# Kernel optimization log

Measured on AMD Instinct MI355X. Metric: run time of the kernel, lower is better.

Reference implementation:

```python
import jax, jax.numpy as jnp
import numpy as np

HIDDEN = 4096
N_HEADS = 16
HEAD_DIM = HIDDEN // N_HEADS  # 256
ROTARY_DIM = 64
MAX_POS = 2048
INIT_RANGE = 0.02


def _create_sinusoidal_positions(num_pos, dim):
    inv_freq = 1.0 / 10000 ** (np.arange(0, dim, 2) / dim)
    sinusoid_inp = np.einsum('i,j->ij', np.arange(num_pos), inv_freq).astype('float32')
    sin, cos = np.sin(sinusoid_inp), np.cos(sinusoid_inp)
    sentinel = dim // 2 + dim % 2
    out = np.zeros((num_pos, dim), dtype=np.float32)
    out[:, :sentinel] = sin
    out[:, sentinel:] = cos
    return jnp.array(out)

EMBED_POSITIONS = _create_sinusoidal_positions(MAX_POS, ROTARY_DIM)  # [MAX_POS, ROTARY_DIM]


def _rotate_every_two(t):
    # t: [B,S,H,R] -> interleaved (-x1, x0, -x3, x2, ...)
    rot = jnp.stack((-t[..., 1::2], t[..., ::2]), axis=-1)
    return rot.reshape(rot.shape[:-2] + (-1,))


def _apply_rotary(t, sin, cos):
    # sin/cos: [B,S,R/2] -> element-wise repeat x2 along last axis -> [B,S,1,R]
    sin_p = jnp.repeat(sin[:, :, None, :], 2, axis=-1)
    cos_p = jnp.repeat(cos[:, :, None, :], 2, axis=-1)
    return t * cos_p + _rotate_every_two(t) * sin_p


def setup_inputs() -> dict:
    key = jax.random.key(0)
    k0, k1, k2, k3, k4 = jax.random.split(key, 5)
    B, S = 2, 2048
    hidden_states = jax.random.normal(k0, (B, S, HIDDEN), dtype=jnp.float32)
    attention_mask = jnp.ones((B, S), dtype=jnp.float32)
    position_ids = jnp.broadcast_to(jnp.arange(S, dtype=jnp.int32), (B, S))
    Wq = jax.random.normal(k1, (HIDDEN, HIDDEN), dtype=jnp.float32) * INIT_RANGE
    Wk = jax.random.normal(k2, (HIDDEN, HIDDEN), dtype=jnp.float32) * INIT_RANGE
    Wv = jax.random.normal(k3, (HIDDEN, HIDDEN), dtype=jnp.float32) * INIT_RANGE
    Wo = jax.random.normal(k4, (HIDDEN, HIDDEN), dtype=jnp.float32) * INIT_RANGE
    return {"hidden_states": hidden_states, "attention_mask": attention_mask,
            "position_ids": position_ids, "Wq": Wq, "Wk": Wk, "Wv": Wv, "Wo": Wo}


def reference(hidden_states, attention_mask, position_ids, Wq, Wk, Wv, Wo):
    B, S, _ = hidden_states.shape
    # QKV projections (no bias), split heads -> [B,S,H,D]
    q = (hidden_states @ Wq).reshape(B, S, N_HEADS, HEAD_DIM)
    k = (hidden_states @ Wk).reshape(B, S, N_HEADS, HEAD_DIM)
    v = (hidden_states @ Wv).reshape(B, S, N_HEADS, HEAD_DIM)

    sincos = jnp.take(EMBED_POSITIONS, position_ids, axis=0)  # [B,S,ROTARY_DIM]
    sin, cos = jnp.split(sincos, 2, axis=-1)

    # Interleaved RoPE on first ROTARY_DIM channels only
    q_rot = _apply_rotary(q[..., :ROTARY_DIM], sin, cos)
    k_rot = _apply_rotary(k[..., :ROTARY_DIM], sin, cos)
    q = jnp.concatenate([q_rot, q[..., ROTARY_DIM:]], axis=-1)
    k = jnp.concatenate([k_rot, k[..., ROTARY_DIM:]], axis=-1)

    # Combined causal + padding mask -> additive bias
    causal = jnp.tril(jnp.ones((S, S), dtype=bool))[None, None]          # [1,1,S,S]
    pad = (attention_mask > 0)[:, None, None, :]                          # [B,1,1,S]
    mask = causal & pad                                                    # [B,1,S,S]
    bias = jnp.where(mask, 0.0, jnp.finfo(jnp.float32).min).astype(jnp.float32)

    # Scaled dot-product attention (query pre-scaled, as in flax dpa_weights)
    q = q / jnp.sqrt(jnp.float32(HEAD_DIM))
    scores = jnp.einsum('bqhd,bkhd->bhqk', q, k) + bias
    attn = jax.nn.softmax(scores, axis=-1)
    out = jnp.einsum('bhqk,bkhd->bqhd', attn, v).reshape(B, S, HIDDEN)
    return out @ Wo
```

## Files before the change

### kernel.cpp

```cpp
#include <hip/hip_runtime.h>


typedef unsigned short u16;
typedef __attribute__((ext_vector_type(4))) float f32x4;
typedef __attribute__((ext_vector_type(8))) short s16x8;
typedef __attribute__((ext_vector_type(4))) unsigned short u16x4;

#define HID 4096
#define SEQ 2048
#define NMAT (4096ull * 4096ull)

__device__ __forceinline__ u16 f2bf(float x) {
  unsigned int u = __builtin_bit_cast(unsigned int, x);
  u += 0x7FFFu + ((u >> 16) & 1u);
  return (u16)(u >> 16);
}
__device__ __forceinline__ float bf2f(u16 x) {
  unsigned int u = ((unsigned int)x) << 16;
  return __builtin_bit_cast(float, u);
}
__device__ __forceinline__ void cp16(const void* g, void* l) {
  __builtin_amdgcn_global_load_lds((__attribute__((address_space(1))) void*)(g),
                                   (__attribute__((address_space(3))) void*)(l),
                                   16, 0, 0);
}

__global__ __launch_bounds__(256) void k_cvt(const float* __restrict__ src,
                                             u16* __restrict__ dst) {
  size_t i = ((size_t)blockIdx.x * 256 + threadIdx.x) * 8;
  f32x4 a = *(const f32x4*)(src + i);
  f32x4 b = *(const f32x4*)(src + i + 4);
  u16x4 o0, o1;
  o0[0] = f2bf(a[0]); o0[1] = f2bf(a[1]); o0[2] = f2bf(a[2]); o0[3] = f2bf(a[3]);
  o1[0] = f2bf(b[0]); o1[1] = f2bf(b[1]); o1[2] = f2bf(b[2]); o1[3] = f2bf(b[3]);
  *(u16x4*)(dst + i) = o0;
  *(u16x4*)(dst + i + 4) = o1;
}

__global__ __launch_bounds__(256) void k_wtrans(const float* __restrict__ W0,
                                                const float* __restrict__ W1,
                                                const float* __restrict__ W2,
                                                const float* __restrict__ W3,
                                                u16* __restrict__ WT) {
  int z = blockIdx.z;
  const float* W = (z == 0) ? W0 : (z == 1) ? W1 : (z == 2) ? W2 : W3;
  u16* T = WT + (size_t)z * NMAT;
  __shared__ u16 tile[64][70];
  int t = threadIdx.x, tx = t & 15, ty = t >> 4;
  int n0 = blockIdx.x * 64, k0 = blockIdx.y * 64;
  for (int i = 0; i < 4; i++) {
    int kl = ty + 16 * i;
    f32x4 v = *(const f32x4*)(W + (size_t)(k0 + kl) * HID + n0 + tx * 4);
    tile[kl][tx * 4 + 0] = f2bf(v[0]);
    tile[kl][tx * 4 + 1] = f2bf(v[1]);
    tile[kl][tx * 4 + 2] = f2bf(v[2]);
    tile[kl][tx * 4 + 3] = f2bf(v[3]);
  }
  __syncthreads();
  for (int i = 0; i < 4; i++) {
    int nl = ty + 16 * i;
    u16x4 o;
    o[0] = tile[tx * 4 + 0][nl];
    o[1] = tile[tx * 4 + 1][nl];
    o[2] = tile[tx * 4 + 2][nl];
    o[3] = tile[tx * 4 + 3][nl];
    *(u16x4*)(T + (size_t)(n0 + nl) * HID + k0 + tx * 4) = o;
  }
}

__global__ __launch_bounds__(256) void k_vtrans(const u16* __restrict__ V,
                                                u16* __restrict__ Vt) {
  int bh = blockIdx.z, b = bh >> 4, h = bh & 15;
  int tok0 = blockIdx.x * 64, d0 = blockIdx.y * 64;
  __shared__ u16 tile[64][70];
  int t = threadIdx.x, tx = t & 15, ty = t >> 4;
  for (int i = 0; i < 4; i++) {
    int tl = ty + 16 * i;
    u16x4 v = *(const u16x4*)(V + (size_t)(b * SEQ + tok0 + tl) * HID + h * 256 + d0 + tx * 4);
    tile[tl][tx * 4 + 0] = v[0];
    tile[tl][tx * 4 + 1] = v[1];
    tile[tl][tx * 4 + 2] = v[2];
    tile[tl][tx * 4 + 3] = v[3];
  }
  __syncthreads();
  for (int i = 0; i < 4; i++) {
    int dl = ty + 16 * i;
    u16x4 o;
    o[0] = tile[tx * 4 + 0][dl];
    o[1] = tile[tx * 4 + 1][dl];
    o[2] = tile[tx * 4 + 2][dl];
    o[3] = tile[tx * 4 + 3][dl];
    *(u16x4*)(Vt + ((size_t)bh * 256 + d0 + dl) * SEQ + tok0 + tx * 4) = o;
  }
}

template <bool QKV>
__global__ __launch_bounds__(256) void k_gemm(const u16* __restrict__ A,
                                              const u16* __restrict__ Bt0,
                                              u16* __restrict__ Cb0,
                                              float* __restrict__ Cf) {
  const int t = threadIdx.x, lane = t & 63, w = t >> 6;
  const int bm = blockIdx.y * 128, bn = blockIdx.x * 128;
  const u16* Bt = Bt0;
  u16* Cb = Cb0;
  float scale = 1.f;
  if (QKV) {
    int z = blockIdx.z;
    Bt += (size_t)z * NMAT;
    Cb += (size_t)z * NMAT;
    if (z == 0) scale = 0.0625f;
  }
  __shared__ u16 As[4096];
  __shared__ u16 Bs[4096];
  int r = t >> 2, cs0 = t & 3, cg = cs0 ^ ((r >> 1) & 3);
  const u16* ga = A + (size_t)(bm + r) * HID + cg * 8;
  const u16* gb = Bt + (size_t)(bn + r) * HID + cg * 8;
  u16* la = As + w * 512;
  u16* lb = Bs + w * 512;
  const int wm = (w >> 1) * 64, wn = (w & 1) * 64;
  const u16* ra[4];
  const u16* rb[4];
  for (int mi = 0; mi < 4; mi++) {
    int row = wm + mi * 16 + (lane & 15);
    int cs = (lane >> 4) ^ ((row >> 1) & 3);
    ra[mi] = As + row * 32 + cs * 8;
  }
  for (int ni = 0; ni < 4; ni++) {
    int row = wn + ni * 16 + (lane & 15);
    int cs = (lane >> 4) ^ ((row >> 1) & 3);
    rb[ni] = Bs + row * 32 + cs * 8;
  }
  f32x4 acc[4][4] = {};
  for (int k0 = 0; k0 < HID; k0 += 32) {
    __syncthreads();
    cp16(ga, la);
    cp16(ga + 64 * HID, la + 2048);
    cp16(gb, lb);
    cp16(gb + 64 * HID, lb + 2048);
    ga += 32;
    gb += 32;
    __syncthreads();
    s16x8 af[4], bf[4];
    for (int mi = 0; mi < 4; mi++) af[mi] = *(const s16x8*)ra[mi];
    for (int ni = 0; ni < 4; ni++) bf[ni] = *(const s16x8*)rb[ni];
    for (int mi = 0; mi < 4; mi++)
      for (int ni = 0; ni < 4; ni++)
        acc[mi][ni] = __builtin_amdgcn_mfma_f32_16x16x32_bf16(af[mi], bf[ni], acc[mi][ni], 0, 0, 0);
  }
  for (int mi = 0; mi < 4; mi++)
    for (int ni = 0; ni < 4; ni++) {
      int ml = bm + wm + mi * 16 + ((lane >> 4) << 2);
      int nl = bn + wn + ni * 16 + (lane & 15);
      for (int rr = 0; rr < 4; rr++) {
        float v = acc[mi][ni][rr];
        if (QKV)
          Cb[(size_t)(ml + rr) * HID + nl] = f2bf(v * scale);
        else
          Cf[(size_t)(ml + rr) * HID + nl] = v;
      }
    }
}

__global__ __launch_bounds__(256) void k_rope(u16* __restrict__ Q, u16* __restrict__ K,
                                              const int* __restrict__ pid) {
  int i = blockIdx.x * 256 + threadIdx.x;
  int m = i >> 9, rem = i & 511, h = rem >> 5, p = rem & 31;
  int pos = pid[m];
  double inv = pow(10000.0, -(double)p / 32.0);
  double ang = (double)pos * inv;
  float sv = (float)sin(ang), cv = (float)cos(ang);
  size_t idx = (size_t)m * HID + h * 256 + 2 * p;
  {
    unsigned int qp = *(const unsigned int*)(Q + idx);
    float a = bf2f((u16)qp), b = bf2f((u16)(qp >> 16));
    unsigned int o = (unsigned int)f2bf(a * cv - b * sv) |
                     ((unsigned int)f2bf(b * cv + a * sv) << 16);
    *(unsigned int*)(Q + idx) = o;
  }
  {
    unsigned int kp = *(const unsigned int*)(K + idx);
    float a = bf2f((u16)kp), b = bf2f((u16)(kp >> 16));
    unsigned int o = (unsigned int)f2bf(a * cv - b * sv) |
                     ((unsigned int)f2bf(b * cv + a * sv) << 16);
    *(unsigned int*)(K + idx) = o;
  }
}

__global__ __launch_bounds__(256, 2) void k_flash(const u16* __restrict__ Q,
                                                  const u16* __restrict__ Kg,
                                                  const u16* __restrict__ Vt,
                                                  const float* __restrict__ am,
                                                  u16* __restrict__ O) {
  __shared__ u16 smem[36864];
  u16* sK = smem;
  u16* sV = smem + 16384;
  u16* sP = smem + 32768;
  const int t = threadIdx.x, lane = t & 63, w = t >> 6;
  const int qt = gridDim.x - 1 - blockIdx.x;
  const int q0 = qt * 64;
  const int bh = blockIdx.y, b = bh >> 4, h = bh & 15;
  const size_t tokb = (size_t)b * SEQ;
  const int ch0 = h * 256;

  for (int j = 0; j < 8; j++) {
    int fc = j * 256 + t;
    int r = fc >> 5, cs = fc & 31, cg = cs ^ (r & 7);
    cp16(Q + (tokb + q0 + r) * (size_t)HID + ch0 + cg * 8, sK + j * 2048 + w * 512);
  }
  __syncthreads();
  s16x8 qf[8];
  {
    int rq = w * 16 + (lane & 15);
    for (int kf = 0; kf < 8; kf++) {
      int cs = ((lane >> 4) + 4 * kf) ^ (rq & 7);
      qf[kf] = *(const s16x8*)(sK + rq * 256 + cs * 8);
    }
  }
  f32x4 oacc[16] = {};
  float mrow[4], lrow[4];
  for (int rr = 0; rr < 4; rr++) { mrow[rr] = -1e30f; lrow[rr] = 0.f; }

  const int ntiles = qt + 1;
  for (int it = 0; it < ntiles; it++) {
    const int kt0 = it * 64;
    __syncthreads();
    for (int j = 0; j < 8; j++) {
      int fc = j * 256 + t;
      int r = fc >> 5, cs = fc & 31, cg = cs ^ (r & 7);
      cp16(Kg + (tokb + kt0 + r) * (size_t)HID + ch0 + cg * 8, sK + j * 2048 + w * 512);
    }
    for (int j = 0; j < 8; j++) {
      int fc = j * 256 + t;
      int rd = fc >> 3, cs = fc & 7, cg = cs ^ (rd & 7);
      cp16(Vt + ((size_t)bh * 256 + rd) * SEQ + kt0 + cg * 8, sV + j * 2048 + w * 512);
    }
    __syncthreads();
    f32x4 sacc[4] = {};
    for (int kf = 0; kf < 8; kf++) {
      s16x8 bf[4];
      for (int ni = 0; ni < 4; ni++) {
        int rk = ni * 16 + (lane & 15);
        int cs = ((lane >> 4) + 4 * kf) ^ (rk & 7);
        bf[ni] = *(const s16x8*)(sK + rk * 256 + cs * 8);
      }
      for (int ni = 0; ni < 4; ni++)
        sacc[ni] = __builtin_amdgcn_mfma_f32_16x16x32_bf16(qf[kf], bf[ni], sacc[ni], 0, 0, 0);
    }
    float amv[4];
    for (int ni = 0; ni < 4; ni++) amv[ni] = am[b * SEQ + kt0 + ni * 16 + (lane & 15)];
    const bool tail = (kt0 + 64 > q0);
    {
      int rbase = q0 + w * 16 + ((lane >> 4) << 2);
      for (int ni = 0; ni < 4; ni++) {
        int colg = kt0 + ni * 16 + (lane & 15);
        bool dead = (amv[ni] <= 0.f);
        for (int rr = 0; rr < 4; rr++)
          if (dead || (tail && colg > rbase + rr)) sacc[ni][rr] = -1e30f;
      }
    }
    float alpha[4];
    for (int rr = 0; rr < 4; rr++) {
      float v = fmaxf(fmaxf(sacc[0][rr], sacc[1][rr]),
                      fmaxf(sacc[2][rr], sacc[3][rr]));
      v = fmaxf(v, __shfl_xor(v, 1));
      v = fmaxf(v, __shfl_xor(v, 2));
      v = fmaxf(v, __shfl_xor(v, 4));
      v = fmaxf(v, __shfl_xor(v, 8));
      float mnew = fmaxf(mrow[rr], v);
      alpha[rr] = __expf(mrow[rr] - mnew);
      mrow[rr] = mnew;
    }
    for (int ni = 0; ni < 4; ni++)
      for (int rr = 0; rr < 4; rr++)
        sacc[ni][rr] = __expf(sacc[ni][rr] - mrow[rr]);
    for (int rr = 0; rr < 4; rr++) {
      float sm = sacc[0][rr] + sacc[1][rr] + sacc[2][rr] + sacc[3][rr];
      sm += __shfl_xor(sm, 1);
      sm += __shfl_xor(sm, 2);
      sm += __shfl_xor(sm, 4);
      sm += __shfl_xor(sm, 8);
      lrow[rr] = lrow[rr] * alpha[rr] + sm;
    }
    for (int nd = 0; nd < 16; nd++)
      for (int rr = 0; rr < 4; rr++) oacc[nd][rr] *= alpha[rr];
    for (int ni = 0; ni < 4; ni++) {
      int ktl = ni * 16 + (lane & 15);
      for (int rr = 0; rr < 4; rr++) {
        int pq = w * 16 + ((lane >> 4) << 2) + rr;
        int cs = (ktl >> 3) ^ (pq & 7);
        sP[pq * 64 + cs * 8 + (ktl & 7)] = f2bf(sacc[ni][rr]);
      }
    }
    for (int kf2 = 0; kf2 < 2; kf2++) {
      s16x8 pa;
      {
        int pq = w * 16 + (lane & 15);
        int cs = ((lane >> 4) + 4 * kf2) ^ (pq & 7);
        pa = *(const s16x8*)(sP + pq * 64 + cs * 8);
      }
      for (int nd = 0; nd < 16; nd++) {
        int rd = nd * 16 + (lane & 15);
        int cs = ((lane >> 4) + 4 * kf2) ^ (rd & 7);
        s16x8 vb = *(const s16x8*)(sV + rd * 64 + cs * 8);
        oacc[nd] = __builtin_amdgcn_mfma_f32_16x16x32_bf16(pa, vb, oacc[nd], 0, 0, 0);
      }
    }
  }
  {
    float rl[4];
    for (int rr = 0; rr < 4; rr++) rl[rr] = (lrow[rr] > 0.f) ? 1.f / lrow[rr] : 0.f;
    for (int nd = 0; nd < 16; nd++)
      for (int rr = 0; rr < 4; rr++) {
        size_t row = tokb + q0 + w * 16 + ((lane >> 4) << 2) + rr;
        O[row * HID + ch0 + nd * 16 + (lane & 15)] = f2bf(oacc[nd][rr] * rl[rr]);
      }
  }
}

extern "C" void kernel_launch(void* const* d_in, const int* in_sizes, int n_in,
                              void* d_out, int out_size, void* d_ws, size_t ws_size,
                              hipStream_t stream) {
  const float* hs = (const float*)d_in[0];
  const float* am = (const float*)d_in[1];
  const int* pid = (const int*)d_in[2];
  const float* Wq = (const float*)d_in[3];
  const float* Wk = (const float*)d_in[4];
  const float* Wv = (const float*)d_in[5];
  const float* Wo = (const float*)d_in[6];
  float* out = (float*)d_out;

  u16* wsp = (u16*)d_ws;
  u16* hsb = wsp;
  u16* WT = wsp + NMAT;
  u16* Qb = wsp + 5 * NMAT;
  u16* Kb = wsp + 6 * NMAT;
  u16* Vb = wsp + 7 * NMAT;
  u16* Vt = wsp + 1 * NMAT;
  u16* attn = hsb;

  k_cvt<<<8192, 256, 0, stream>>>(hs, hsb);
  k_wtrans<<<dim3(64, 64, 4), 256, 0, stream>>>(Wq, Wk, Wv, Wo, WT);
  k_gemm<true><<<dim3(32, 32, 3), 256, 0, stream>>>(hsb, WT, Qb, nullptr);
  k_rope<<<8192, 256, 0, stream>>>(Qb, Kb, pid);
  k_vtrans<<<dim3(32, 4, 32), 256, 0, stream>>>(Vb, Vt);
  k_flash<<<dim3(32, 32), 256, 0, stream>>>(Qb, Kb, Vt, am, attn);
  k_gemm<false><<<dim3(32, 32, 1), 256, 0, stream>>>(attn, WT + 3 * NMAT, nullptr, out);
}
```

Before: 1.239 ms.

## Replace GEMM with 256x256-tile 8-wave double-buffered pipelined kernel

Rewrites the projection GEMM kernel to use 256x256 output tiles computed by 8 waves. It double-buffers 64-wide k-slices in 128 KB of LDS, loading with async global-to-LDS copies and a swizzled layout. Loads, barriers and MFMA phases are interleaved with priority hints, so global memory latency overlaps with matrix math. A block-index swizzle improves L2 reuse. The cost is higher LDS and register use, which limits occupancy to one large block per CU.

Measured after the change: 1.032 ms. 1.2x faster.

```diff
diff --git a/kernel.cpp b/kernel.cpp
--- a/kernel.cpp
+++ b/kernel.cpp
@@ -95,12 +95,18 @@
 }
 
 template <bool QKV>
-__global__ __launch_bounds__(256) void k_gemm(const u16* __restrict__ A,
-                                              const u16* __restrict__ Bt0,
-                                              u16* __restrict__ Cb0,
-                                              float* __restrict__ Cf) {
+__global__ __launch_bounds__(512, 2) void k_gemm8(const u16* __restrict__ A,
+                                                  const u16* __restrict__ Bt0,
+                                                  u16* __restrict__ Cb0,
+                                                  float* __restrict__ Cf) {
+  __shared__ u16 lds[65536];
+  char* lds8 = (char*)lds;
   const int t = threadIdx.x, lane = t & 63, w = t >> 6;
-  const int bm = blockIdx.y * 128, bn = blockIdx.x * 128;
+  const int wm = w >> 2, wn = w & 3;
+  const int l15 = lane & 15, g = lane >> 4;
+  int lin = blockIdx.y * 16 + blockIdx.x;
+  int swz = (lin & 7) * 32 + (lin >> 3);
+  const int bm = (swz >> 4) * 256, bn = (swz & 15) * 256;
   const u16* Bt = Bt0;
   u16* Cb = Cb0;
   float scale = 1.f;
@@ -110,47 +116,83 @@
     Cb += (size_t)z * NMAT;
     if (z == 0) scale = 0.0625f;
   }
-  __shared__ u16 As[4096];
-  __shared__ u16 Bs[4096];
-  int r = t >> 2, cs0 = t & 3, cg = cs0 ^ ((r >> 1) & 3);
-  const u16* ga = A + (size_t)(bm + r) * HID + cg * 8;
-  const u16* gb = Bt + (size_t)(bn + r) * HID + cg * 8;
-  u16* la = As + w * 512;
-  u16* lb = Bs + w * 512;
-  const int wm = (w >> 1) * 64, wn = (w & 1) * 64;
-  const u16* ra[4];
-  const u16* rb[4];
-  for (int mi = 0; mi < 4; mi++) {
-    int row = wm + mi * 16 + (lane & 15);
-    int cs = (lane >> 4) ^ ((row >> 1) & 3);
-    ra[mi] = As + row * 32 + cs * 8;
-  }
-  for (int ni = 0; ni < 4; ni++) {
-    int row = wn + ni * 16 + (lane & 15);
-    int cs = (lane >> 4) ^ ((row >> 1) & 3);
-    rb[ni] = Bs + row * 32 + cs * 8;
-  }
-  f32x4 acc[4][4] = {};
-  for (int k0 = 0; k0 < HID; k0 += 32) {
-    __syncthreads();
-    cp16(ga, la);
-    cp16(ga + 64 * HID, la + 2048);
-    cp16(gb, lb);
-    cp16(gb + 64 * HID, lb + 2048);
-    ga += 32;
-    gb += 32;
-    __syncthreads();
-    s16x8 af[4], bf[4];
-    for (int mi = 0; mi < 4; mi++) af[mi] = *(const s16x8*)ra[mi];
-    for (int ni = 0; ni < 4; ni++) bf[ni] = *(const s16x8*)rb[ni];
-    for (int mi = 0; mi < 4; mi++)
-      for (int ni = 0; ni < 4; ni++)
-        acc[mi][ni] = __builtin_amdgcn_mfma_f32_16x16x32_bf16(af[mi], bf[ni], acc[mi][ni], 0, 0, 0);
-  }
-  for (int mi = 0; mi < 4; mi++)
+  const int Px = (t * 16) ^ (((t >> 5) & 1) << 5);
+  const int r_s = Px >> 6, c_s = (Px & 63) >> 1;
+  const u16* gA0 = A + (size_t)(bm + r_s) * HID + c_s;
+  const u16* gA1 = gA0 + 128ull * HID;
+  const u16* gB0 = Bt + (size_t)(bn + r_s) * HID + c_s;
+  const u16* gB1 = gB0 + 128ull * HID;
+  char* stA = lds8 + w * 1024;
+  char* stB = lds8 + 32768 + w * 1024;
+  const int sb = ((l15 >> 3) & 1) << 5;
+  const int aL0 = wm * 16384 + ((l15 * 64 + g * 16) ^ sb);
+  const int bL0 = 32768 + (wn >> 1) * 16384 + ((((wn & 1) * 64 + l15) * 64 + g * 16) ^ sb);
+  const int aL1 = aL0 + 65536, bL1 = bL0 + 65536;
+
+  f32x4 acc[8][4] = {};
+  s16x8 af[4][2], b0[2][2], b1[2][2];
+
+#define STG(P, D, KT) { const u16* s_ = (P) + (size_t)(KT) * 64; \
+                        cp16(s_, (D)); cp16(s_ + 32, (D) + 8192); }
+#define LDA8(MH, AL) \
+  _Pragma("unroll") for (int mi = 0; mi < 4; mi++) { \
+    af[mi][0] = *(const s16x8*)(lds8 + (AL) + (MH) * 4096 + mi * 1024); \
+    af[mi][1] = *(const s16x8*)(lds8 + (AL) + (MH) * 4096 + mi * 1024 + 8192); }
+#define LDB8(BQ, NH, BL) \
+  _Pragma("unroll") for (int n2 = 0; n2 < 2; n2++) { \
+    BQ[n2][0] = *(const s16x8*)(lds8 + (BL) + ((NH) * 2 + n2) * 1024); \
+    BQ[n2][1] = *(const s16x8*)(lds8 + (BL) + ((NH) * 2 + n2) * 1024 + 8192); }
+#define MM8(MH, BQ, NH) \
+  _Pragma("unroll") for (int mi = 0; mi < 4; mi++) \
+  _Pragma("unroll") for (int n2 = 0; n2 < 2; n2++) { \
+    acc[(MH)*4+mi][(NH)*2+n2] = __builtin_amdgcn_mfma_f32_16x16x32_bf16( \
+        af[mi][0], BQ[n2][0], acc[(MH)*4+mi][(NH)*2+n2], 0, 0, 0); \
+    acc[(MH)*4+mi][(NH)*2+n2] = __builtin_amdgcn_mfma_f32_16x16x32_bf16( \
+        af[mi][1], BQ[n2][1], acc[(MH)*4+mi][(NH)*2+n2], 0, 0, 0); }
+#define BAR() __builtin_amdgcn_s_barrier()
+#define LGKM0() asm volatile("s_waitcnt lgkmcnt(0)" ::: "memory")
+#define PRIO1() __builtin_amdgcn_s_setprio(1)
+#define PRIO0() __builtin_amdgcn_s_setprio(0)
+
+  STG(gB0, stB, 0); STG(gB1, stB + 16384, 0);
+  STG(gA0, stA, 0); STG(gA1, stA + 16384, 0);
+  STG(gB0, stB + 65536, 1); STG(gB1, stB + 65536 + 16384, 1);
+  asm volatile("s_waitcnt vmcnt(4)" ::: "memory");
+  BAR();
+
+  for (int it = 0; it < 32; ++it) {
+    const int k1 = 2 * it + 1;
+    const int k2 = (2 * it + 2 < 64) ? 2 * it + 2 : 63;
+    const int k3 = (2 * it + 3 < 64) ? 2 * it + 3 : 63;
+    LDA8(0, aL0); LDB8(b0, 0, bL0); STG(gA0, stA + 65536, k1);
+    BAR(); LGKM0(); PRIO1(); MM8(0, b0, 0); PRIO0(); BAR();
+    LDB8(b1, 1, bL0); STG(gA1, stA + 65536 + 16384, k1);
+    BAR(); LGKM0(); PRIO1(); MM8(0, b1, 1); PRIO0(); BAR();
+    LDA8(1, aL0); STG(gB0, stB, k2);
+    BAR(); LGKM0(); PRIO1(); MM8(1, b1, 1); PRIO0(); BAR();
+    STG(gB1, stB + 16384, k2);
+    BAR(); PRIO1(); MM8(1, b0, 0); PRIO0();
+    asm volatile("s_waitcnt vmcnt(4)" ::: "memory");
+    BAR();
+    LDA8(0, aL1); LDB8(b0, 0, bL1); STG(gA0, stA, k2);
+    BAR(); LGKM0(); PRIO1(); MM8(0, b0, 0); PRIO0(); BAR();
+    LDB8(b1, 1, bL1); STG(gA1, stA + 16384, k2);
+    BAR(); LGKM0(); PRIO1(); MM8(0, b1, 1); PRIO0(); BAR();
+    LDA8(1, aL1); STG(gB0, stB + 65536, k3);
+    BAR(); LGKM0(); PRIO1(); MM8(1, b1, 1); PRIO0(); BAR();
+    STG(gB1, stB + 65536 + 16384, k3);
+    BAR(); PRIO1(); MM8(1, b0, 0); PRIO0();
+    asm volatile("s_waitcnt vmcnt(4)" ::: "memory");
+    BAR();
+  }
+  asm volatile("s_waitcnt vmcnt(0)" ::: "memory");
+#pragma unroll
+  for (int mi = 0; mi < 8; mi++)
+#pragma unroll
     for (int ni = 0; ni < 4; ni++) {
-      int ml = bm + wm + mi * 16 + ((lane >> 4) << 2);
-      int nl = bn + wn + ni * 16 + (lane & 15);
+      const int ml = bm + wm * 128 + mi * 16 + g * 4;
+      const int nl = bn + wn * 64 + ni * 16 + l15;
+#pragma unroll
       for (int rr = 0; rr < 4; rr++) {
         float v = acc[mi][ni][rr];
         if (QKV)
@@ -159,6 +201,14 @@
           Cf[(size_t)(ml + rr) * HID + nl] = v;
       }
     }
+#undef STG
+#undef LDA8
+#undef LDB8
+#undef MM8
+#undef BAR
+#undef LGKM0
+#undef PRIO1
+#undef PRIO0
 }
 
 __global__ __launch_bounds__(256) void k_rope(u16* __restrict__ Q, u16* __restrict__ K,
@@ -340,9 +390,9 @@
 
   k_cvt<<<8192, 256, 0, stream>>>(hs, hsb);
   k_wtrans<<<dim3(64, 64, 4), 256, 0, stream>>>(Wq, Wk, Wv, Wo, WT);
-  k_gemm<true><<<dim3(32, 32, 3), 256, 0, stream>>>(hsb, WT, Qb, nullptr);
+  k_gemm8<true><<<dim3(16, 16, 3), 512, 0, stream>>>(hsb, WT, Qb, nullptr);
   k_rope<<<8192, 256, 0, stream>>>(Qb, Kb, pid);
   k_vtrans<<<dim3(32, 4, 32), 256, 0, stream>>>(Vb, Vt);
   k_flash<<<dim3(32, 32), 256, 0, stream>>>(Qb, Kb, Vt, am, attn);
-  k_gemm<false><<<dim3(32, 32, 1), 256, 0, stream>>>(attn, WT + 3 * NMAT, nullptr, out);
-}
+  k_gemm8<false><<<dim3(16, 16, 1), 512, 0, stream>>>(attn, WT + 3 * NMAT, nullptr, out);
+}
```
